# Performance work log

Measured on AMD Instinct MI355X. Metric: run time of the kernel, lower is better.

Reference implementation:

```python
import jax, jax.numpy as jnp
import numpy as np

B, N, C = 16, 1024, 768
NUM_HEADS = 8
HEAD_DIM = C // NUM_HEADS
TEMP_INIT = 0.05
EPS_NORM = 1e-12   # F.normalize eps
EPS_LN = 1e-5      # LayerNorm eps


def setup_inputs() -> dict:
    key = jax.random.key(0)
    ks = jax.random.split(key, 4)
    x = jax.random.normal(ks[0], (B, N, C), dtype=jnp.float32)
    w_qkv = jax.random.normal(ks[1], (3 * C, C), dtype=jnp.float32) * (1.0 / np.sqrt(C))
    w_proj = jax.random.normal(ks[2], (C, C), dtype=jnp.float32) * (1.0 / np.sqrt(C))
    temperature = jnp.ones((NUM_HEADS, 1, 1), dtype=jnp.float32) * TEMP_INIT
    conv_w = jax.random.normal(ks[3], (C, 1, 3, 3), dtype=jnp.float32) * (1.0 / 3.0)
    gamma = jnp.ones((C,), dtype=jnp.float32)
    beta = jnp.zeros((C,), dtype=jnp.float32)
    return {"x": x, "w_qkv": w_qkv, "w_proj": w_proj, "temperature": temperature,
            "conv_w": conv_w, "gamma": gamma, "beta": beta, "H": 32, "W": 32}


def _l2norm_tokens(t):
    # normalize along token dim (axis=-2), matching F.normalize(dim=-2)
    n = jnp.sqrt(jnp.sum(t * t, axis=-2, keepdims=True))
    return t / jnp.maximum(n, EPS_NORM)


def reference(x, w_qkv, w_proj, temperature, conv_w, gamma, beta, H, W):
    b, n, c = x.shape
    h, d = NUM_HEADS, HEAD_DIM
    qkv = (x @ w_qkv.T).reshape(b, n, 3, h, d).transpose(2, 0, 3, 1, 4)  # [3,B,h,N,d]
    q, k, v = qkv[0], qkv[1], qkv[2]
    q = _l2norm_tokens(q)
    k = _l2norm_tokens(k)
    # cross-covariance attention over channels: [B,h,d,d]
    A = jnp.einsum('bhnd,bhne->bhde', q, k) / temperature[None]
    A = jax.nn.softmax(A, axis=-1)
    # v @ A^T : [B,h,N,d]
    x_xca = jnp.einsum('bhne,bhde->bhnd', v, A)
    x_xca = x_xca.transpose(0, 2, 1, 3).reshape(b, n, c)
    x_xca = x_xca @ w_proj.T
    # depthwise 3x3 local propagation
    x_img = x.transpose(0, 2, 1).reshape(b, c, H, W)
    x_local = jax.lax.conv_general_dilated(
        x_img, conv_w, window_strides=(1, 1), padding=((1, 1), (1, 1)),
        dimension_numbers=('NCHW', 'OIHW', 'NCHW'), feature_group_count=c)
    x_local = x_local.reshape(b, c, n).transpose(0, 2, 1)
    y = x_xca + 0.1 * x_local
    mu = jnp.mean(y, axis=-1, keepdims=True)
    var = jnp.mean((y - mu) ** 2, axis=-1, keepdims=True)
    return (y - mu) * jax.lax.rsqrt(var + EPS_LN) * gamma + beta
```

## Files before the change

### kernel.cpp

```cpp
#include <hip/hip_runtime.h>

#define DEVI __device__ __forceinline__

typedef __bf16 bf16x8 __attribute__((ext_vector_type(8)));
typedef float f32x4 __attribute__((ext_vector_type(4)));

DEVI unsigned short f2bf(float f) {
  unsigned u = __builtin_bit_cast(unsigned, f);
  u += 0x7FFFu + ((u >> 16) & 1u);
  return (unsigned short)(u >> 16);
}
DEVI float bf2f(unsigned short s) {
  return __builtin_bit_cast(float, ((unsigned)s) << 16);
}
DEVI f32x4 mfma16(bf16x8 a, bf16x8 b, f32x4 c) {
  return __builtin_amdgcn_mfma_f32_16x16x32_bf16(a, b, c, 0, 0, 0);
}
DEVI void gload16(const void* g, void* l) {
  __builtin_amdgcn_global_load_lds(
      (const __attribute__((address_space(1))) void*)g,
      (__attribute__((address_space(3))) void*)l, 16, 0, 0);
}
template <int ROWB>
DEVI bf16x8 frag_ld(const char* lds, int row, int kb) {
  int off = row * ROWB + (kb ^ ((row & 7) << 4));
  return __builtin_bit_cast(bf16x8, *(const uint4*)(lds + off));
}

__global__ __launch_bounds__(256) void k_cvt2(const float* __restrict__ a,
                                              unsigned short* __restrict__ oa, int n4a,
                                              const float* __restrict__ b,
                                              unsigned short* __restrict__ ob, int n4b) {
  const int tid = threadIdx.x;
  if (blockIdx.x < 2048) {
    const int chunk = (blockIdx.x & 7) * 256 + (blockIdx.x >> 3);
    const int i0 = chunk * 1536;
    for (int i = i0 + tid; i < i0 + 1536; i += 256) {
      float4 f = ((const float4*)a)[i];
      ushort4 o;
      o.x = f2bf(f.x); o.y = f2bf(f.y); o.z = f2bf(f.z); o.w = f2bf(f.w);
      ((ushort4*)oa)[i] = o;
    }
  } else {
    for (int i = (blockIdx.x - 2048) * 256 + tid; i < n4b; i += 256 * 256) {
      float4 f = ((const float4*)b)[i];
      ushort4 o;
      o.x = f2bf(f.x); o.y = f2bf(f.y); o.z = f2bf(f.z); o.w = f2bf(f.w);
      ((ushort4*)ob)[i] = o;
    }
  }
}

template <int MODE>
DEVI void gemm_body(char* lds, const unsigned short* __restrict__ A,
                    const unsigned short* __restrict__ B0,
                    unsigned short* __restrict__ o0, unsigned short* __restrict__ o1,
                    unsigned short* __restrict__ o2, float* __restrict__ ns) {
  const int tid = threadIdx.x, l = tid & 63, wid = tid >> 6;
  const int wr = wid >> 2, wc = wid & 3;
  const int xg = blockIdx.x;
  const int CPX = MODE ? 64 : 192;
  const int NJT = MODE ? 4 : 12;
  const int li = (xg & 7) * CPX + (xg >> 3);
  const int jt = li % NJT, mt = li / NJT;
  const int m0 = mt * 128, j0 = jt * 192;
  const unsigned short* Bb = MODE ? B0 + (size_t)(m0 >> 10) * 589824 : B0;

  const unsigned short* srcg[4][2];
  int ldso[4][2];
#pragma unroll
  for (int sg = 0; sg < 4; ++sg) {
    const bool isA = (sg == 0) || (sg == 3);
#pragma unroll
    for (int i = 0; i < 2; ++i) {
      int c;
      if (sg == 0)      c = (wid < 4) ? wid : wid + 4;
      else if (sg == 3) c = (wid < 4) ? wid + 4 : wid + 8;
      else if (sg == 1) { int cc = 2 * wid + i; c = (cc >> 2) * 6 + (cc & 3); }
      else              c = (wid >> 1) * 6 + 4 + (wid & 1);
      const int r0 = 8 * c;
      const int r = r0 + (l >> 3);
      const int scol = ((l & 7) ^ (l >> 3)) << 3;
      srcg[sg][i] = (isA ? A + (size_t)(m0 + r) * 768 : Bb + (size_t)(j0 + r) * 768) + scol;
      ldso[sg][i] = (isA ? 0 : 16384) + r0 * 128;
    }
  }
  const int swz = (l & 7) << 4;
  const int uu = (l >> 4) << 4;
  const int c0 = uu ^ swz;
  const int c1 = (64 | uu) ^ swz;
  const int arow = (wr * 64 + (l & 15)) * 128;
  const int brow = 16384 + (wc * 48 + (l & 15)) * 128;

  f32x4 acc[4][3];
#pragma unroll
  for (int i = 0; i < 4; ++i)
#pragma unroll
    for (int j = 0; j < 3; ++j)
#pragma unroll
      for (int e = 0; e < 4; ++e) acc[i][j][e] = 0.f;
  bf16x8 a[2][2], a2[2][2], b01[2][2], b2[2];

#define STAGE1(sg, nxt, ko) \
  gload16(srcg[sg][0] + (ko), lds + (nxt)*40960 + ldso[sg][0])
#define STAGE2(sg, nxt, ko)                                        \
  do {                                                             \
    gload16(srcg[sg][0] + (ko), lds + (nxt)*40960 + ldso[sg][0]);  \
    gload16(srcg[sg][1] + (ko), lds + (nxt)*40960 + ldso[sg][1]);  \
  } while (0)
#define LD128(off) __builtin_bit_cast(bf16x8, *(const uint4*)(cb_ + (off)))

  STAGE1(0, 0, 0); STAGE2(1, 0, 0); STAGE1(2, 0, 0); STAGE1(3, 0, 0);
  asm volatile("s_waitcnt vmcnt(2)" ::: "memory");
  __builtin_amdgcn_s_barrier();

#define KBODY(KT, LASTF)                                                              \
  {                                                                                   \
    const char* cb_ = lds + ((KT) & 1) * 40960;                                       \
    const int nxt = (((KT) & 1) ^ 1);                                                 \
    const int ko = ((KT) + 1) * 64;                                                   \
    _Pragma("unroll") for (int mf = 0; mf < 2; ++mf) {                                \
      a[mf][0] = LD128(arow + mf * 2048 + c0);                                        \
      a[mf][1] = LD128(arow + mf * 2048 + c1);                                        \
    }                                                                                 \
    _Pragma("unroll") for (int nf = 0; nf < 2; ++nf) {                                \
      b01[nf][0] = LD128(brow + nf * 2048 + c0);                                      \
      b01[nf][1] = LD128(brow + nf * 2048 + c1);                                      \
    }                                                                                 \
    if (!(LASTF)) {                                                                   \
      STAGE1(0, nxt, ko); STAGE2(1, nxt, ko);                                         \
      asm volatile("s_waitcnt vmcnt(3)" ::: "memory");                                \
    } else {                                                                          \
      asm volatile("s_waitcnt vmcnt(0)" ::: "memory");                                \
    }                                                                                 \
    __builtin_amdgcn_s_barrier();                                                     \
    __builtin_amdgcn_s_setprio(1);                                                    \
    _Pragma("unroll") for (int mf = 0; mf < 2; ++mf)                                  \
      _Pragma("unroll") for (int nf = 0; nf < 2; ++nf) {                              \
        acc[mf][nf] = mfma16(a[mf][0], b01[nf][0], acc[mf][nf]);                      \
        acc[mf][nf] = mfma16(a[mf][1], b01[nf][1], acc[mf][nf]);                      \
      }                                                                               \
    __builtin_amdgcn_s_setprio(0);                                                    \
    b2[0] = LD128(brow + 2 * 2048 + c0);                                              \
    b2[1] = LD128(brow + 2 * 2048 + c1);                                              \
    _Pragma("unroll") for (int mf = 0; mf < 2; ++mf) {                                \
      a2[mf][0] = LD128(arow + (mf + 2) * 2048 + c0);                                 \
      a2[mf][1] = LD128(arow + (mf + 2) * 2048 + c1);                                 \
    }                                                                                 \
    if (!(LASTF)) {                                                                   \
      STAGE1(2, nxt, ko); STAGE1(3, nxt, ko);                                         \
      asm volatile("s_waitcnt vmcnt(2)" ::: "memory");                                \
    }                                                                                 \
    __builtin_amdgcn_s_barrier();                                                     \
    __builtin_amdgcn_s_setprio(1);                                                    \
    _Pragma("unroll") for (int mf = 0; mf < 2; ++mf) {                                \
      acc[mf][2] = mfma16(a[mf][0], b2[0], acc[mf][2]);                               \
      acc[mf][2] = mfma16(a[mf][1], b2[1], acc[mf][2]);                               \
    }                                                                                 \
    _Pragma("unroll") for (int mf = 0; mf < 2; ++mf)                                  \
      _Pragma("unroll") for (int nf = 0; nf < 2; ++nf) {                              \
        acc[mf + 2][nf] = mfma16(a2[mf][0], b01[nf][0], acc[mf + 2][nf]);             \
        acc[mf + 2][nf] = mfma16(a2[mf][1], b01[nf][1], acc[mf + 2][nf]);             \
      }                                                                               \
    _Pragma("unroll") for (int mf = 0; mf < 2; ++mf) {                                \
      acc[mf + 2][2] = mfma16(a2[mf][0], b2[0], acc[mf + 2][2]);                      \
      acc[mf + 2][2] = mfma16(a2[mf][1], b2[1], acc[mf + 2][2]);                      \
    }                                                                                 \
    __builtin_amdgcn_s_setprio(0);                                                    \
  }

#pragma unroll 1
  for (int kt = 0; kt < 11; ++kt) KBODY(kt, false);
  KBODY(11, true);
#undef KBODY
#undef STAGE2
#undef STAGE1
#undef LD128

  if constexpr (MODE == 0) {
    const int s = j0 / 768;
    const int jin0 = (j0 % 768) + wc * 48 + (l & 15);
    const int ntok0 = m0 + wr * 64 + ((l >> 4) << 2);
    const int bb = m0 >> 10;
#pragma unroll
    for (int mf = 0; mf < 4; ++mf) {
      const int nt = ntok0 + mf * 16;
      const int nin = nt & 1023;
#pragma unroll
      for (int nf = 0; nf < 3; ++nf) {
        const int jj = jin0 + nf * 16;
        const int hh = jj / 96, dd = jj % 96;
        if (s == 2) {
          unsigned short* vp = o2 + (size_t)nt * 768 + jj;
#pragma unroll
          for (int rr = 0; rr < 4; ++rr) vp[rr * 768] = f2bf(acc[mf][nf][rr]);
        } else {
          unsigned short* base = (s == 0) ? o0 : o1;
          ushort4 pk;
          pk.x = f2bf(acc[mf][nf][0]); pk.y = f2bf(acc[mf][nf][1]);
          pk.z = f2bf(acc[mf][nf][2]); pk.w = f2bf(acc[mf][nf][3]);
          *(ushort4*)(base + ((size_t)((bb * 8 + hh) * 96 + dd)) * 1024 + nin) = pk;
        }
      }
    }
    if (s < 2) {
      float* nsp = (s == 0) ? ns : ns + 12288;
#pragma unroll
      for (int nf = 0; nf < 3; ++nf) {
        float ss = 0.f;
#pragma unroll
        for (int mf = 0; mf < 4; ++mf)
#pragma unroll
          for (int rr = 0; rr < 4; ++rr) ss += acc[mf][nf][rr] * acc[mf][nf][rr];
        ss += __shfl_xor(ss, 16, 64);
        ss += __shfl_xor(ss, 32, 64);
        if ((l >> 4) == 0) {
          const int jj = jin0 + nf * 16;
          atomicAdd(&nsp[(bb * 8 + jj / 96) * 96 + jj % 96], ss);
        }
      }
    }
  } else {
    unsigned short* t = (unsigned short*)lds;
    const int nl0 = wr * 64 + ((l >> 4) << 2);
    const int cl0 = wc * 48 + (l & 15);
#pragma unroll
    for (int mf = 0; mf < 4; ++mf)
#pragma unroll
      for (int nf = 0; nf < 3; ++nf)
#pragma unroll
        for (int rr = 0; rr < 4; ++rr)
          t[(nl0 + mf * 16 + rr) * 200 + cl0 + nf * 16] = f2bf(acc[mf][nf][rr]);
    __builtin_amdgcn_s_barrier();
    for (int i2 = tid; i2 < 3072; i2 += 512) {
      int r = i2 / 24, ch = i2 % 24;
      uint4 u = *(const uint4*)(t + r * 200 + ch * 8);
      *(uint4*)(o0 + (size_t)(m0 + r) * 768 + j0 + ch * 8) = u;
    }
  }
}

__global__ __launch_bounds__(512, 4) void kg0_qkv(const unsigned short* __restrict__ A,
                                                  const unsigned short* __restrict__ B0,
                                                  unsigned short* __restrict__ o0,
                                                  unsigned short* __restrict__ o1,
                                                  unsigned short* __restrict__ o2,
                                                  float* __restrict__ ns) {
  __shared__ alignas(16) char lds[81920];
  gemm_body<0>(lds, A, B0, o0, o1, o2, ns);
}
__global__ __launch_bounds__(512, 4) void kg1_proj(const unsigned short* __restrict__ A,
                                                   const unsigned short* __restrict__ B0,
                                                   unsigned short* __restrict__ o0) {
  __shared__ alignas(16) char lds[81920];
  gemm_body<1>(lds, A, B0, o0, nullptr, nullptr, nullptr);
}

__global__ __launch_bounds__(256) void k_qk(const unsigned short* __restrict__ qT,
                                            const unsigned short* __restrict__ kT,
                                            float* __restrict__ PA) {
  __shared__ alignas(16) char lQK[2][24576];
  const int blk = blockIdx.x, tid = threadIdx.x, lane = tid & 63, wid = tid >> 6;
  const int bh = blk >> 1, kh = blk & 1;
  const int wr = wid >> 1, wc = wid & 1;
  const unsigned short* qb = qT + (size_t)bh * 96 * 1024 + kh * 512;
  const unsigned short* kb = kT + (size_t)bh * 96 * 1024 + kh * 512;

  const unsigned short* srcp[6];
  int dsto[6];
#pragma unroll
  for (int i = 0; i < 6; ++i) {
    int cid = wid * 6 + i;
    bool isK = cid >= 12;
    int c = isK ? cid - 12 : cid;
    int p = c * 1024 + lane * 16;
    int r = p >> 7, cb = p & 127;
    int cbs = cb ^ ((r & 7) << 4);
    srcp[i] = (isK ? kb : qb) + (size_t)r * 1024 + (cbs >> 1);
    dsto[i] = (isK ? 12288 : 0) + c * 1024;
  }

  f32x4 acc[3][3];
#pragma unroll
  for (int i = 0; i < 3; ++i)
#pragma unroll
    for (int j = 0; j < 3; ++j)
#pragma unroll
      for (int e = 0; e < 4; ++e) acc[i][j][e] = 0.f;

#pragma unroll
  for (int i = 0; i < 6; ++i) gload16(srcp[i], lQK[0] + dsto[i]);
  asm volatile("s_waitcnt vmcnt(0)" ::: "memory");
  __builtin_amdgcn_s_barrier();

#pragma unroll 1
  for (int kt = 0; kt < 8; ++kt) {
    const char* bq = lQK[kt & 1];
    if (kt < 7) {
      char* nb = lQK[(kt + 1) & 1];
      const int ko = (kt + 1) * 64;
#pragma unroll
      for (int i = 0; i < 6; ++i) gload16(srcp[i] + ko, nb + dsto[i]);
    }
#pragma unroll
    for (int ks = 0; ks < 2; ++ks) {
      const int kb2 = ks * 64 + ((lane >> 4) << 4);
      bf16x8 af[3], bfv[3];
#pragma unroll
      for (int mb = 0; mb < 3; ++mb) af[mb] = frag_ld<128>(bq, wr * 48 + mb * 16 + (lane & 15), kb2);
#pragma unroll
      for (int nb2 = 0; nb2 < 3; ++nb2) bfv[nb2] = frag_ld<128>(bq + 12288, wc * 48 + nb2 * 16 + (lane & 15), kb2);
#pragma unroll
      for (int mb = 0; mb < 3; ++mb)
#pragma unroll
        for (int nb2 = 0; nb2 < 3; ++nb2) acc[mb][nb2] = mfma16(af[mb], bfv[nb2], acc[mb][nb2]);
    }
    asm volatile("s_waitcnt vmcnt(0)" ::: "memory");
    __builtin_amdgcn_s_barrier();
  }

  float* pa = PA + (size_t)(bh * 2 + kh) * 9216;
  const int rb = wr * 48 + ((lane >> 4) << 2);
  const int eb = wc * 48 + (lane & 15);
#pragma unroll
  for (int mb = 0; mb < 3; ++mb)
#pragma unroll
    for (int nb = 0; nb < 3; ++nb)
#pragma unroll
      for (int rr = 0; rr < 4; ++rr)
        pa[(rb + mb * 16 + rr) * 96 + eb + nb * 16] = acc[mb][nb][rr];
}

__global__ __launch_bounds__(256) void k_soft(const float* __restrict__ PA,
                                              const float* __restrict__ ns,
                                              const float* __restrict__ temp,
                                              unsigned short* __restrict__ PT) {
  __shared__ float aa[9216];
  __shared__ unsigned short ptb[96 * 104];
  __shared__ float lrq[96], lrk[96];
  const int bh = blockIdx.x, tid = threadIdx.x, lane = tid & 63, wid = tid >> 6;
  const float invt = 1.f / temp[bh & 7];
  if (tid < 96)       lrq[tid] = 1.f / fmaxf(sqrtf(ns[bh * 96 + tid]), 1e-12f);
  else if (tid < 192) lrk[tid - 96] = 1.f / fmaxf(sqrtf(ns[12288 + bh * 96 + tid - 96]), 1e-12f);

  const float4* pp = (const float4*)(PA + (size_t)bh * 2 * 9216);
  for (int i = tid; i < 2304; i += 256) {
    float4 x0 = pp[i], x1 = pp[i + 2304];
    float4 r;
    r.x = x0.x + x1.x; r.y = x0.y + x1.y; r.z = x0.z + x1.z; r.w = x0.w + x1.w;
    ((float4*)aa)[i] = r;
  }
  __syncthreads();

  for (int d = wid; d < 96; d += 4) {
    float v0 = aa[d * 96 + lane] * lrq[d] * lrk[lane] * invt;
    float v1 = (lane < 32) ? aa[d * 96 + 64 + lane] * lrq[d] * lrk[64 + lane] * invt : -3.0e38f;
    float mx = fmaxf(v0, v1);
#pragma unroll
    for (int off = 32; off; off >>= 1) mx = fmaxf(mx, __shfl_xor(mx, off, 64));
    float p0 = __expf(v0 - mx);
    float p1 = (lane < 32) ? __expf(v1 - mx) : 0.f;
    float ssum = p0 + p1;
#pragma unroll
    for (int off = 32; off; off >>= 1) ssum += __shfl_xor(ssum, off, 64);
    float rs = 1.f / ssum;
    ptb[lane * 104 + d] = f2bf(p0 * rs);
    if (lane < 32) ptb[(64 + lane) * 104 + d] = f2bf(p1 * rs);
  }
  __syncthreads();
  for (int i = tid; i < 1152; i += 256) {
    int r = i / 12, ch = i % 12;
    *(uint4*)(PT + (size_t)bh * 9216 + r * 96 + ch * 8) = *(const uint4*)(ptb + r * 104 + ch * 8);
  }
}

__global__ __launch_bounds__(256) void k_prep(const unsigned short* __restrict__ PT,
                                              const float* __restrict__ wproj,
                                              unsigned short* __restrict__ B_all) {
  __shared__ alignas(16) char pl[19968 + 39936];
  unsigned short* lPt = (unsigned short*)pl;
  unsigned short* lW  = (unsigned short*)(pl + 19968);
  unsigned short* tr  = lW;
  const int blk = blockIdx.x;
  const int idx = blk >> 3;
  const int b = (blk & 7) * 2 + (idx >> 5);
  const int h = (idx >> 2) & 7, cq = idx & 3;
  const int tid = threadIdx.x, l = tid & 63, wid = tid >> 6;
  const int wr = wid >> 1, wc = wid & 1;

  const unsigned short* pt = PT + (size_t)(b * 8 + h) * 96 * 96;
  for (int i2 = tid; i2 < 1152; i2 += 256) {
    int r = i2 / 12, ch = i2 % 12;
    *(uint4*)(lPt + r * 104 + ch * 8) = *(const uint4*)(pt + r * 96 + ch * 8);
  }
  for (int i2 = tid; i2 < 4608; i2 += 256) {
    int r = i2 / 24, ch = i2 % 24;
    float4 f = *(const float4*)(wproj + (size_t)(cq * 192 + r) * 768 + h * 96 + ch * 4);
    ushort4 o;
    o.x = f2bf(f.x); o.y = f2bf(f.y); o.z = f2bf(f.z); o.w = f2bf(f.w);
    *(ushort4*)(lW + r * 104 + ch * 4) = o;
  }
  __syncthreads();

  f32x4 acc[3][6];
#pragma unroll
  for (int i = 0; i < 3; ++i)
#pragma unroll
    for (int j = 0; j < 6; ++j)
#pragma unroll
      for (int e = 0; e < 4; ++e) acc[i][j][e] = 0.f;

#pragma unroll
  for (int ks = 0; ks < 3; ++ks) {
    const int kof = ks * 32 + ((l >> 4) << 3);
    bf16x8 af[3], bv[6];
#pragma unroll
    for (int mb = 0; mb < 3; ++mb)
      af[mb] = __builtin_bit_cast(bf16x8, *(const uint4*)(lPt + (wr * 48 + mb * 16 + (l & 15)) * 104 + kof));
#pragma unroll
    for (int nb = 0; nb < 6; ++nb)
      bv[nb] = __builtin_bit_cast(bf16x8, *(const uint4*)(lW + (wc * 96 + nb * 16 + (l & 15)) * 104 + kof));
#pragma unroll
    for (int mb = 0; mb < 3; ++mb)
#pragma unroll
      for (int nb = 0; nb < 6; ++nb) acc[mb][nb] = mfma16(af[mb], bv[nb], acc[mb][nb]);
  }

  __syncthreads();
  const int e0 = wr * 48 + ((l >> 4) << 2);
  const int cl0 = wc * 96 + (l & 15);
#pragma unroll
  for (int mb = 0; mb < 3; ++mb)
#pragma unroll
    for (int nb = 0; nb < 6; ++nb) {
      ushort4 pk;
      pk.x = f2bf(acc[mb][nb][0]); pk.y = f2bf(acc[mb][nb][1]);
      pk.z = f2bf(acc[mb][nb][2]); pk.w = f2bf(acc[mb][nb][3]);
      *(ushort4*)(tr + (cl0 + nb * 16) * 100 + e0 + mb * 16) = pk;
    }
  __syncthreads();
  for (int i2 = tid; i2 < 2304; i2 += 256) {
    int r = i2 / 12, ch = i2 % 12;
    uint4 u = *(const uint4*)(tr + r * 100 + ch * 8);
    *(uint4*)(B_all + ((size_t)(b * 768) + cq * 192 + r) * 768 + h * 96 + ch * 8) = u;
  }
}

__global__ __launch_bounds__(256) void k_final(const unsigned short* __restrict__ yp,
                                               const unsigned short* __restrict__ xb16,
                                               const float* __restrict__ cw,
                                               const float* __restrict__ gamma,
                                               const float* __restrict__ beta,
                                               float* __restrict__ out) {
  const int wid = threadIdx.x >> 6, lane = threadIdx.x & 63;
  const int m = (blockIdx.x & 7) * 2048 + (blockIdx.x >> 3) * 4 + wid;
  const int bb = m >> 10, n = m & 1023, yy = n >> 5, xx = n & 31;
  const unsigned short* xb = xb16 + (size_t)bb * 1024 * 768;

  float yv[3][4];
#pragma unroll
  for (int g = 0; g < 3; ++g) {
    const int c = g * 256 + lane * 4;
    float w36[36];
    const float4* wp = (const float4*)(cw + (size_t)c * 9);
#pragma unroll
    for (int i = 0; i < 9; ++i) *(float4*)(w36 + i * 4) = wp[i];

    float a0 = 0.f, a1 = 0.f, a2 = 0.f, a3 = 0.f;
#pragma unroll
    for (int dy = -1; dy <= 1; ++dy) {
      int ny = yy + dy;
      if ((unsigned)ny < 32u) {
#pragma unroll
        for (int dx = -1; dx <= 1; ++dx) {
          int nx = xx + dx;
          if ((unsigned)nx < 32u) {
            ushort4 v = *(const ushort4*)(xb + (size_t)(ny * 32 + nx) * 768 + c);
            const int j = (dy + 1) * 3 + (dx + 1);
            a0 += w36[0 * 9 + j] * bf2f(v.x);
            a1 += w36[1 * 9 + j] * bf2f(v.y);
            a2 += w36[2 * 9 + j] * bf2f(v.z);
            a3 += w36[3 * 9 + j] * bf2f(v.w);
          }
        }
      }
    }
    ushort4 f = *(const ushort4*)(yp + (size_t)m * 768 + c);
    yv[g][0] = bf2f(f.x) + 0.1f * a0;
    yv[g][1] = bf2f(f.y) + 0.1f * a1;
    yv[g][2] = bf2f(f.z) + 0.1f * a2;
    yv[g][3] = bf2f(f.w) + 0.1f * a3;
  }

  float s1 = 0.f, s2 = 0.f;
#pragma unroll
  for (int g = 0; g < 3; ++g)
#pragma unroll
    for (int e = 0; e < 4; ++e) { s1 += yv[g][e]; s2 += yv[g][e] * yv[g][e]; }
#pragma unroll
  for (int off = 32; off; off >>= 1) {
    s1 += __shfl_xor(s1, off, 64);
    s2 += __shfl_xor(s2, off, 64);
  }
  const float mu = s1 * (1.f / 768.f);
  const float var = s2 * (1.f / 768.f) - mu * mu;
  const float rs = rsqrtf(var + 1e-5f);

#pragma unroll
  for (int g = 0; g < 3; ++g) {
    const int c = g * 256 + lane * 4;
    float4 gm = *(const float4*)(gamma + c);
    float4 bt = *(const float4*)(beta + c);
    float4 o;
    o.x = (yv[g][0] - mu) * rs * gm.x + bt.x;
    o.y = (yv[g][1] - mu) * rs * gm.y + bt.y;
    o.z = (yv[g][2] - mu) * rs * gm.z + bt.z;
    o.w = (yv[g][3] - mu) * rs * gm.w + bt.w;
    *(float4*)(out + (size_t)m * 768 + c) = o;
  }
}

extern "C" void kernel_launch(void* const* d_in, const int* in_sizes, int n_in,
                              void* d_out, int out_size, void* d_ws, size_t ws_size,
                              hipStream_t stream) {
  const float* x     = (const float*)d_in[0];
  const float* wqkv  = (const float*)d_in[1];
  const float* wproj = (const float*)d_in[2];
  const float* temp  = (const float*)d_in[3];
  const float* cw    = (const float*)d_in[4];
  const float* gamma = (const float*)d_in[5];
  const float* beta  = (const float*)d_in[6];
  float* out = (float*)d_out;
  char* ws = (char*)d_ws;

  unsigned short* xb    = (unsigned short*)(ws);
  unsigned short* wqb   = (unsigned short*)(ws + 25165824);
  unsigned short* PT    = wqb;
  unsigned short* qT    = (unsigned short*)(ws + 28704768);
  unsigned short* yp    = qT;
  unsigned short* kT    = (unsigned short*)(ws + 53870592);
  unsigned short* B_all = kT;
  unsigned short* vP    = (unsigned short*)(ws + 79036416);
  float* ns             = (float*)(ws + 104202240);
  float* PA             = (float*)(ws + 104300544);

  hipMemsetAsync(ns, 0, 98304, stream);
  k_cvt2<<<dim3(2304), dim3(256), 0, stream>>>(x, xb, 16384 * 768 / 4,
                                               wqkv, wqb, 2304 * 768 / 4);
  kg0_qkv<<<dim3(1536), dim3(512), 0, stream>>>(xb, wqb, qT, kT, vP, ns);
  k_qk<<<dim3(256), dim3(256), 0, stream>>>(qT, kT, PA);
  k_soft<<<dim3(128), dim3(256), 0, stream>>>(PA, ns, temp, PT);
  k_prep<<<dim3(512), dim3(256), 0, stream>>>(PT, wproj, B_all);
  kg1_proj<<<dim3(512), dim3(512), 0, stream>>>(vP, B_all, yp);
  k_final<<<dim3(4096), dim3(256), 0, stream>>>(yp, xb, cw, gamma, beta, out);
}
```

Before: 209.8 us.

## Move norm sums into QK kernel and fuse softmax into prep kernel

The token-axis sum of squares for q and k is no longer taken in the QKV GEMM epilogue with atomics. It is now taken in the QK kernel from the bf16 fragments already loaded into registers. The separate softmax kernel is merged into k_prep, so each prep block recomputes the softmax for its (b,h) straight into LDS, and the global PT round trip and one launch go away. The cost is that softmax is computed redundantly four times per head. The norms also now come from bf16-rounded q and k rather than the fp32 accumulators, which slightly changes numerics.

```diff
diff --git a/kernel.cpp b/kernel.cpp
--- a/kernel.cpp
+++ b/kernel.cpp
@@ -26,6 +26,18 @@
   int off = row * ROWB + (kb ^ ((row & 7) << 4));
   return __builtin_bit_cast(bf16x8, *(const uint4*)(lds + off));
 }
+DEVI float ssq8(uint4 u) {
+  unsigned a[4] = {u.x, u.y, u.z, u.w};
+  float s = 0.f;
+#pragma unroll
+  for (int i = 0; i < 4; ++i) {
+    float lo = __builtin_bit_cast(float, a[i] << 16);
+    float hi = __builtin_bit_cast(float, a[i] & 0xFFFF0000u);
+    s += lo * lo + hi * hi;
+  }
+  return s;
+}
+DEVI float ssqbf8(bf16x8 v) { return ssq8(__builtin_bit_cast(uint4, v)); }
 
 __global__ __launch_bounds__(256) void k_cvt2(const float* __restrict__ a,
                                               unsigned short* __restrict__ oa, int n4a,
@@ -55,7 +67,7 @@
 DEVI void gemm_body(char* lds, const unsigned short* __restrict__ A,
                     const unsigned short* __restrict__ B0,
                     unsigned short* __restrict__ o0, unsigned short* __restrict__ o1,
-                    unsigned short* __restrict__ o2, float* __restrict__ ns) {
+                    unsigned short* __restrict__ o2) {
   const int tid = threadIdx.x, l = tid & 63, wid = tid >> 6;
   const int wr = wid >> 2, wc = wid & 3;
   const int xg = blockIdx.x;
@@ -148,7 +160,7 @@
       a2[mf][1] = LD128(arow + (mf + 2) * 2048 + c1);                                 \
     }                                                                                 \
     if (!(LASTF)) {                                                                   \
-      STAGE1(2, nxt, ko); STAGE1(3, nxt, ko);                                         \
+      STAGE1(2, nxt, ko); STAGE1(3, nxt, ko);                                        \
       asm volatile("s_waitcnt vmcnt(2)" ::: "memory");                                \
     }                                                                                 \
     __builtin_amdgcn_s_barrier();                                                     \
@@ -203,23 +215,6 @@
         }
       }
     }
-    if (s < 2) {
-      float* nsp = (s == 0) ? ns : ns + 12288;
-#pragma unroll
-      for (int nf = 0; nf < 3; ++nf) {
-        float ss = 0.f;
-#pragma unroll
-        for (int mf = 0; mf < 4; ++mf)
-#pragma unroll
-          for (int rr = 0; rr < 4; ++rr) ss += acc[mf][nf][rr] * acc[mf][nf][rr];
-        ss += __shfl_xor(ss, 16, 64);
-        ss += __shfl_xor(ss, 32, 64);
-        if ((l >> 4) == 0) {
-          const int jj = jin0 + nf * 16;
-          atomicAdd(&nsp[(bb * 8 + jj / 96) * 96 + jj % 96], ss);
-        }
-      }
-    }
   } else {
     unsigned short* t = (unsigned short*)lds;
     const int nl0 = wr * 64 + ((l >> 4) << 2);
@@ -244,21 +239,21 @@
                                                   const unsigned short* __restrict__ B0,
                                                   unsigned short* __restrict__ o0,
                                                   unsigned short* __restrict__ o1,
-                                                  unsigned short* __restrict__ o2,
-                                                  float* __restrict__ ns) {
+                                                  unsigned short* __restrict__ o2) {
   __shared__ alignas(16) char lds[81920];
-  gemm_body<0>(lds, A, B0, o0, o1, o2, ns);
+  gemm_body<0>(lds, A, B0, o0, o1, o2);
 }
 __global__ __launch_bounds__(512, 4) void kg1_proj(const unsigned short* __restrict__ A,
                                                    const unsigned short* __restrict__ B0,
                                                    unsigned short* __restrict__ o0) {
   __shared__ alignas(16) char lds[81920];
-  gemm_body<1>(lds, A, B0, o0, nullptr, nullptr, nullptr);
+  gemm_body<1>(lds, A, B0, o0, nullptr, nullptr);
 }
 
 __global__ __launch_bounds__(256) void k_qk(const unsigned short* __restrict__ qT,
                                             const unsigned short* __restrict__ kT,
-                                            float* __restrict__ PA) {
+                                            float* __restrict__ PA,
+                                            float* __restrict__ ns) {
   __shared__ alignas(16) char lQK[2][24576];
   const int blk = blockIdx.x, tid = threadIdx.x, lane = tid & 63, wid = tid >> 6;
   const int bh = blk >> 1, kh = blk & 1;
@@ -287,6 +282,7 @@
     for (int j = 0; j < 3; ++j)
 #pragma unroll
       for (int e = 0; e < 4; ++e) acc[i][j][e] = 0.f;
+  float sq[3] = {0.f, 0.f, 0.f}, sk[3] = {0.f, 0.f, 0.f};
 
 #pragma unroll
   for (int i = 0; i < 6; ++i) gload16(srcp[i], lQK[0] + dsto[i]);
@@ -310,6 +306,14 @@
       for (int mb = 0; mb < 3; ++mb) af[mb] = frag_ld<128>(bq, wr * 48 + mb * 16 + (lane & 15), kb2);
 #pragma unroll
       for (int nb2 = 0; nb2 < 3; ++nb2) bfv[nb2] = frag_ld<128>(bq + 12288, wc * 48 + nb2 * 16 + (lane & 15), kb2);
+      if (wc == 0) {
+#pragma unroll
+        for (int mb = 0; mb < 3; ++mb) sq[mb] += ssqbf8(af[mb]);
+      }
+      if (wr == 0) {
+#pragma unroll
+        for (int nb2 = 0; nb2 < 3; ++nb2) sk[nb2] += ssqbf8(bfv[nb2]);
+      }
 #pragma unroll
       for (int mb = 0; mb < 3; ++mb)
 #pragma unroll
@@ -329,17 +333,49 @@
 #pragma unroll
       for (int rr = 0; rr < 4; ++rr)
         pa[(rb + mb * 16 + rr) * 96 + eb + nb * 16] = acc[mb][nb][rr];
-}
-
-__global__ __launch_bounds__(256) void k_soft(const float* __restrict__ PA,
+
+  if (wc == 0) {
+#pragma unroll
+    for (int mb = 0; mb < 3; ++mb) {
+      float s = sq[mb];
+      s += __shfl_xor(s, 16, 64);
+      s += __shfl_xor(s, 32, 64);
+      if ((lane >> 4) == 0)
+        atomicAdd(&ns[bh * 96 + wr * 48 + mb * 16 + (lane & 15)], s);
+    }
+  }
+  if (wr == 0) {
+#pragma unroll
+    for (int nb2 = 0; nb2 < 3; ++nb2) {
+      float s = sk[nb2];
+      s += __shfl_xor(s, 16, 64);
+      s += __shfl_xor(s, 32, 64);
+      if ((lane >> 4) == 0)
+        atomicAdd(&ns[12288 + bh * 96 + wc * 48 + nb2 * 16 + (lane & 15)], s);
+    }
+  }
+}
+
+__global__ __launch_bounds__(256) void k_prep(const float* __restrict__ PA,
                                               const float* __restrict__ ns,
                                               const float* __restrict__ temp,
-                                              unsigned short* __restrict__ PT) {
-  __shared__ float aa[9216];
-  __shared__ unsigned short ptb[96 * 104];
+                                              const float* __restrict__ wproj,
+                                              unsigned short* __restrict__ B_all) {
+  __shared__ alignas(16) char pl[19968 + 39936];
+  unsigned short* lPt = (unsigned short*)pl;
+  float* aa = (float*)(pl + 19968);
+  unsigned short* lW = (unsigned short*)(pl + 19968);
+  unsigned short* tr = lW;
   __shared__ float lrq[96], lrk[96];
-  const int bh = blockIdx.x, tid = threadIdx.x, lane = tid & 63, wid = tid >> 6;
-  const float invt = 1.f / temp[bh & 7];
+  const int blk = blockIdx.x;
+  const int idx = blk >> 3;
+  const int b = (blk & 7) * 2 + (idx >> 5);
+  const int h = (idx >> 2) & 7, cq = idx & 3;
+  const int bh = b * 8 + h;
+  const int tid = threadIdx.x, l = tid & 63, wid = tid >> 6;
+  const int wr = wid >> 1, wc = wid & 1;
+  const float invt = 1.f / temp[h];
+
   if (tid < 96)       lrq[tid] = 1.f / fmaxf(sqrtf(ns[bh * 96 + tid]), 1e-12f);
   else if (tid < 192) lrk[tid - 96] = 1.f / fmaxf(sqrtf(ns[12288 + bh * 96 + tid - 96]), 1e-12f);
 
@@ -353,46 +389,22 @@
   __syncthreads();
 
   for (int d = wid; d < 96; d += 4) {
-    float v0 = aa[d * 96 + lane] * lrq[d] * lrk[lane] * invt;
-    float v1 = (lane < 32) ? aa[d * 96 + 64 + lane] * lrq[d] * lrk[64 + lane] * invt : -3.0e38f;
+    float v0 = aa[d * 96 + l] * lrq[d] * lrk[l] * invt;
+    float v1 = (l < 32) ? aa[d * 96 + 64 + l] * lrq[d] * lrk[64 + l] * invt : -3.0e38f;
     float mx = fmaxf(v0, v1);
 #pragma unroll
     for (int off = 32; off; off >>= 1) mx = fmaxf(mx, __shfl_xor(mx, off, 64));
     float p0 = __expf(v0 - mx);
-    float p1 = (lane < 32) ? __expf(v1 - mx) : 0.f;
+    float p1 = (l < 32) ? __expf(v1 - mx) : 0.f;
     float ssum = p0 + p1;
 #pragma unroll
     for (int off = 32; off; off >>= 1) ssum += __shfl_xor(ssum, off, 64);
     float rs = 1.f / ssum;
-    ptb[lane * 104 + d] = f2bf(p0 * rs);
-    if (lane < 32) ptb[(64 + lane) * 104 + d] = f2bf(p1 * rs);
+    lPt[l * 104 + d] = f2bf(p0 * rs);
+    if (l < 32) lPt[(64 + l) * 104 + d] = f2bf(p1 * rs);
   }
   __syncthreads();
-  for (int i = tid; i < 1152; i += 256) {
-    int r = i / 12, ch = i % 12;
-    *(uint4*)(PT + (size_t)bh * 9216 + r * 96 + ch * 8) = *(const uint4*)(ptb + r * 104 + ch * 8);
-  }
-}
-
-__global__ __launch_bounds__(256) void k_prep(const unsigned short* __restrict__ PT,
-                                              const float* __restrict__ wproj,
-                                              unsigned short* __restrict__ B_all) {
-  __shared__ alignas(16) char pl[19968 + 39936];
-  unsigned short* lPt = (unsigned short*)pl;
-  unsigned short* lW  = (unsigned short*)(pl + 19968);
-  unsigned short* tr  = lW;
-  const int blk = blockIdx.x;
-  const int idx = blk >> 3;
-  const int b = (blk & 7) * 2 + (idx >> 5);
-  const int h = (idx >> 2) & 7, cq = idx & 3;
-  const int tid = threadIdx.x, l = tid & 63, wid = tid >> 6;
-  const int wr = wid >> 1, wc = wid & 1;
-
-  const unsigned short* pt = PT + (size_t)(b * 8 + h) * 96 * 96;
-  for (int i2 = tid; i2 < 1152; i2 += 256) {
-    int r = i2 / 12, ch = i2 % 12;
-    *(uint4*)(lPt + r * 104 + ch * 8) = *(const uint4*)(pt + r * 96 + ch * 8);
-  }
+
   for (int i2 = tid; i2 < 4608; i2 += 256) {
     int r = i2 / 24, ch = i2 % 24;
     float4 f = *(const float4*)(wproj + (size_t)(cq * 192 + r) * 768 + h * 96 + ch * 4);
@@ -535,7 +547,6 @@
 
   unsigned short* xb    = (unsigned short*)(ws);
   unsigned short* wqb   = (unsigned short*)(ws + 25165824);
-  unsigned short* PT    = wqb;
   unsigned short* qT    = (unsigned short*)(ws + 28704768);
   unsigned short* yp    = qT;
   unsigned short* kT    = (unsigned short*)(ws + 53870592);
@@ -547,10 +558,9 @@
   hipMemsetAsync(ns, 0, 98304, stream);
   k_cvt2<<<dim3(2304), dim3(256), 0, stream>>>(x, xb, 16384 * 768 / 4,
                                                wqkv, wqb, 2304 * 768 / 4);
-  kg0_qkv<<<dim3(1536), dim3(512), 0, stream>>>(xb, wqb, qT, kT, vP, ns);
-  k_qk<<<dim3(256), dim3(256), 0, stream>>>(qT, kT, PA);
-  k_soft<<<dim3(128), dim3(256), 0, stream>>>(PA, ns, temp, PT);
-  k_prep<<<dim3(512), dim3(256), 0, stream>>>(PT, wproj, B_all);
+  kg0_qkv<<<dim3(1536), dim3(512), 0, stream>>>(xb, wqb, qT, kT, vP);
+  k_qk<<<dim3(256), dim3(256), 0, stream>>>(qT, kT, PA, ns);
+  k_prep<<<dim3(512), dim3(256), 0, stream>>>(PA, ns, temp, wproj, B_all);
   kg1_proj<<<dim3(512), dim3(512), 0, stream>>>(vP, B_all, yp);
   k_final<<<dim3(4096), dim3(256), 0, stream>>>(yp, xb, cw, gamma, beta, out);
 }
```

Result: faster. 203.5 us (-3.0%).
